# Kernel tuning notes

Hardware: AMD Instinct MI355X
Metric: run time of the kernel (lower is better)

## Reference

```python
import jax, jax.numpy as jnp
import numpy as np

N = 50000          # nodes
E = 500000         # edges (before self-loops)
G = 64             # graphs in batch
SC = 96            # scalar features
D = 32             # embedding dim
IN_DIM = SC + 5 * D  # 256
C = 128            # hidden_channels
H1 = 4             # heads in conv1
NUM_CLASSES = 5
V_OP, V_SRC, V_SINK, V_STR, V_PAY = 256, 512, 512, 128, 1024


def setup_inputs() -> dict:
    key = jax.random.key(0)
    ks = jax.random.split(key, 32)
    inp = {}
    inp['x_scalar'] = jax.random.normal(ks[0], (N, SC), jnp.float32)
    inp['x_opcode'] = jax.random.randint(ks[1], (N, 16), 0, V_OP)
    inp['x_source'] = jax.random.randint(ks[2], (N, 8), 0, V_SRC)
    inp['x_sink'] = jax.random.randint(ks[3], (N, 8), 0, V_SINK)
    inp['x_string_manip'] = jax.random.randint(ks[4], (N, 8), 0, V_STR)
    inp['x_payload'] = jax.random.randint(ks[5], (N, 8), 0, V_PAY)
    inp['edge_index'] = jax.random.randint(ks[6], (2, E), 0, N)
    # sorted graph ids with every graph non-empty
    inp['batch'] = (jnp.arange(N) * G) // N
    # learned params
    s = 0.05
    inp['emb_opcode'] = jax.random.normal(ks[7], (V_OP, D), jnp.float32)
    inp['emb_source'] = jax.random.normal(ks[8], (V_SRC, D), jnp.float32)
    inp['emb_sink'] = jax.random.normal(ks[9], (V_SINK, D), jnp.float32)
    inp['emb_string'] = jax.random.normal(ks[10], (V_STR, D), jnp.float32)
    inp['emb_payload'] = jax.random.normal(ks[11], (V_PAY, D), jnp.float32)
    inp['ln_g'] = jnp.ones((IN_DIM,), jnp.float32)
    inp['ln_b'] = jnp.zeros((IN_DIM,), jnp.float32)
    inp['W1'] = jax.random.normal(ks[12], (IN_DIM, H1 * C), jnp.float32) * s
    inp['att_src1'] = jax.random.normal(ks[13], (H1, C), jnp.float32) * s
    inp['att_dst1'] = jax.random.normal(ks[14], (H1, C), jnp.float32) * s
    inp['b1'] = jnp.zeros((H1 * C,), jnp.float32)
    inp['W2'] = jax.random.normal(ks[15], (H1 * C, C), jnp.float32) * s
    inp['att_src2'] = jax.random.normal(ks[16], (1, C), jnp.float32) * s
    inp['att_dst2'] = jax.random.normal(ks[17], (1, C), jnp.float32) * s
    inp['b2'] = jnp.zeros((C,), jnp.float32)
    inp['Wc1'] = jax.random.normal(ks[18], (C, C // 2), jnp.float32) * s
    inp['bc1'] = jnp.zeros((C // 2,), jnp.float32)
    inp['Wc2'] = jax.random.normal(ks[19], (C // 2, NUM_CLASSES), jnp.float32) * s
    inp['bc2'] = jnp.zeros((NUM_CLASSES,), jnp.float32)
    return inp


def _emb_feat(table, idx):
    # masked mean over the list dim; index 0 is padding
    e = table[idx]                                  # [N, L, D]
    mask = (idx != 0)[..., None].astype(e.dtype)    # [N, L, 1]
    return (e * mask).sum(1) / (mask.sum(1) + 1e-9)


def _layernorm(x, g, b, eps=1e-5):
    mu = x.mean(-1, keepdims=True)
    var = ((x - mu) ** 2).mean(-1, keepdims=True)
    return (x - mu) * jax.lax.rsqrt(var + eps) * g + b


def _gat_conv(x, W, att_src, att_dst, bias, src, dst, heads, out_ch, concat):
    n = x.shape[0]
    h = (x @ W).reshape(n, heads, out_ch)              # [N,H,C]
    a_src = (h * att_src).sum(-1)                      # [N,H]
    a_dst = (h * att_dst).sum(-1)                      # [N,H]
    e = jax.nn.leaky_relu(a_src[src] + a_dst[dst], 0.2)  # [E,H]
    m = jax.ops.segment_max(e, dst, num_segments=n)
    e = jnp.exp(e - m[dst])
    denom = jax.ops.segment_sum(e, dst, num_segments=n)
    alpha = e / (denom[dst] + 1e-16)                   # segment softmax over in-edges
    msg = h[src] * alpha[:, :, None]                   # [E,H,C]
    out = jax.ops.segment_sum(msg, dst, num_segments=n)  # [N,H,C]
    out = out.reshape(n, heads * out_ch) if concat else out.mean(1)
    return out + bias


def reference(x_scalar, x_opcode, x_source, x_sink, x_string_manip, x_payload,
              edge_index, batch,
              emb_opcode, emb_source, emb_sink, emb_string, emb_payload,
              ln_g, ln_b, W1, att_src1, att_dst1, b1,
              W2, att_src2, att_dst2, b2, Wc1, bc1, Wc2, bc2):
    n = x_scalar.shape[0]
    feats = jnp.concatenate([
        x_scalar,
        _emb_feat(emb_opcode, x_opcode),
        _emb_feat(emb_source, x_source),
        _emb_feat(emb_sink, x_sink),
        _emb_feat(emb_string, x_string_manip),
        _emb_feat(emb_payload, x_payload),
    ], axis=1)
    feats = _layernorm(feats, ln_g, ln_b)
    # add self loops (PyG GATConv default)
    loop = jnp.arange(n)
    src = jnp.concatenate([edge_index[0], loop])
    dst = jnp.concatenate([edge_index[1], loop])
    x = jax.nn.elu(_gat_conv(feats, W1, att_src1, att_dst1, b1, src, dst, H1, C, True))
    x = jax.nn.elu(_gat_conv(x, W2, att_src2, att_dst2, b2, src, dst, 1, C, True))
    # global max pool per graph (dropout layers are identity at inference)
    xp = jax.ops.segment_max(x, batch, num_segments=G)  # [G,C]
    hcls = jax.nn.relu(xp @ Wc1 + bc1)
    return hcls @ Wc2 + bc2
```

## Files before the change

### kernel.cpp

```cpp
#include <hip/hip_runtime.h>
#include <hip/hip_bf16.h>
#include <float.h>


#define LEAKY(e) ((e) > 0.f ? (e) : 0.2f * (e))
#define POOL_CH 32

typedef _Float16 half8 __attribute__((ext_vector_type(8)));
typedef float floatx4 __attribute__((ext_vector_type(4)));

__device__ __forceinline__ void async_copy16(const _Float16* gsrc,
                                             const _Float16* ldst) {
  __builtin_amdgcn_global_load_lds(
      (const __attribute__((address_space(1))) unsigned int*)gsrc,
      (__attribute__((address_space(3))) unsigned int*)ldst, 16, 0, 0);
}

__global__ __launch_bounds__(256, 4) void setup_kernel(
    const int* __restrict__ e_dst, int* __restrict__ deg, int E, int HB,
    const float* __restrict__ W1, _Float16* __restrict__ Wt1,
    const float* __restrict__ W2, _Float16* __restrict__ Wt2, int TB,
    const float* __restrict__ xs, const int* __restrict__ xo,
    const int* __restrict__ xsrc, const int* __restrict__ xsk,
    const int* __restrict__ xst, const int* __restrict__ xp,
    const float* __restrict__ eo, const float* __restrict__ es,
    const float* __restrict__ ek, const float* __restrict__ et,
    const float* __restrict__ ep, const float* __restrict__ lng,
    const float* __restrict__ lnb, _Float16* __restrict__ feats, int n) {
  int b = blockIdx.x;
  if (b < HB) {
    int t = b * 256 + threadIdx.x;
    if (t < E) atomicAdd(&deg[e_dst[t]], 1);
    return;
  }
  if (b < HB + TB) {
    int t = (b - HB) * 256 + threadIdx.x;
    if (t < 256 * 512) {
      int nn = t / 256, k = t - nn * 256;
      Wt1[t] = (_Float16)W1[(size_t)k * 512 + nn];
    } else {
      int u = t - 256 * 512;
      int nn = u / 512, k = u - nn * 512;
      Wt2[u] = (_Float16)W2[(size_t)k * 128 + nn];
    }
    return;
  }
  int node = (b - HB - TB) * 4 + (threadIdx.x >> 6);
  if (node >= n) return;
  int l = threadIdx.x & 63;

  int myidx = 0;
  if (l < 16)      myidx = xo[node * 16 + l];
  else if (l < 24) myidx = xsrc[node * 8 + (l - 16)];
  else if (l < 32) myidx = xsk[node * 8 + (l - 24)];
  else if (l < 40) myidx = xst[node * 8 + (l - 32)];
  else if (l < 48) myidx = xp[node * 8 + (l - 40)];

  const float* xrow = xs + (size_t)node * 96;
  float v0 = xrow[l];
  float sc = xrow[64 + (l & 31)];
  float v1, v2, v3;
  bool hi = (l >= 32);
  int d = l & 31;

  {
    float s = 0.f, c = 0.f;
#pragma unroll
    for (int j = 0; j < 16; j++) {
      int id = __shfl(myidx, j);
      float v = eo[(size_t)id * 32 + d];
      float msk = (id != 0) ? 1.f : 0.f;
      s = fmaf(v, msk, s);
      c += msk;
    }
    v1 = hi ? (s / (c + 1e-9f)) : sc;
  }
  {
    const float* tab = hi ? ek : es;
    int base = hi ? 24 : 16;
    float s = 0.f, c = 0.f;
#pragma unroll
    for (int j = 0; j < 8; j++) {
      int id = __shfl(myidx, base + j);
      float v = tab[(size_t)id * 32 + d];
      float msk = (id != 0) ? 1.f : 0.f;
      s = fmaf(v, msk, s);
      c += msk;
    }
    v2 = s / (c + 1e-9f);
  }
  {
    const float* tab = hi ? ep : et;
    int base = hi ? 40 : 32;
    float s = 0.f, c = 0.f;
#pragma unroll
    for (int j = 0; j < 8; j++) {
      int id = __shfl(myidx, base + j);
      float v = tab[(size_t)id * 32 + d];
      float msk = (id != 0) ? 1.f : 0.f;
      s = fmaf(v, msk, s);
      c += msk;
    }
    v3 = s / (c + 1e-9f);
  }

  float sum = v0 + v1 + v2 + v3;
  for (int o = 32; o; o >>= 1) sum += __shfl_xor(sum, o);
  float mu = sum * (1.f / 256.f);
  float d0 = v0 - mu, d1 = v1 - mu, d2 = v2 - mu, d3 = v3 - mu;
  float q = d0 * d0 + d1 * d1 + d2 * d2 + d3 * d3;
  for (int o = 32; o; o >>= 1) q += __shfl_xor(q, o);
  float rstd = rsqrtf(q * (1.f / 256.f) + 1e-5f);

  _Float16* frow = feats + (size_t)node * 256;
  frow[l]       = (_Float16)(d0 * rstd * lng[l] + lnb[l]);
  frow[64 + l]  = (_Float16)(d1 * rstd * lng[64 + l] + lnb[64 + l]);
  frow[128 + l] = (_Float16)(d2 * rstd * lng[128 + l] + lnb[128 + l]);
  frow[192 + l] = (_Float16)(d3 * rstd * lng[192 + l] + lnb[192 + l]);
}

__global__ __launch_bounds__(256) void scan_a(const int* __restrict__ deg,
                                              int* __restrict__ rowptr,
                                              int* __restrict__ bsum, int n) {
  __shared__ int sh[256];
  int b = blockIdx.x, t = threadIdx.x;
  int i = b * 256 + t;
  int v = (i < n) ? deg[i] + 1 : 0;
  sh[t] = v;
  __syncthreads();
  int x = v;
  for (int o = 1; o < 256; o <<= 1) {
    int y = (t >= o) ? sh[t - o] : 0;
    __syncthreads();
    x += y;
    sh[t] = x;
    __syncthreads();
  }
  if (i < n) rowptr[i] = x - v;
  if (t == 255) bsum[b] = x;
}

__global__ __launch_bounds__(256) void scan_c(int* __restrict__ rowptr,
                                              int* __restrict__ rowptr_work,
                                              const int* __restrict__ bsum,
                                              int n, int total) {
  int b = blockIdx.x;
  int off = 0;
  for (int j = 0; j < b; j++) off += bsum[j];
  int i = b * 256 + threadIdx.x;
  if (i < n) {
    int r = rowptr[i] + off;
    rowptr[i] = r;
    rowptr_work[i] = r;
  } else if (i == n) {
    rowptr[n] = total;
  }
}

__global__ __launch_bounds__(256) void fill_kernel(
    const int* __restrict__ src, const int* __restrict__ dst,
    const int* __restrict__ rowptr, int* __restrict__ rowptr_work,
    int* __restrict__ csr_src, int E, int n) {
  int t = blockIdx.x * 256 + threadIdx.x;
  if (t < E) {
    int d = dst[t];
    int pos = atomicAdd(&rowptr_work[d], 1);
    csr_src[pos] = src[t];
  } else if (t < E + n) {
    int i = t - E;
    csr_src[rowptr[i + 1] - 1] = i;
  }
}

__global__ __launch_bounds__(256) void gemm_f16_att(
    const _Float16* __restrict__ A, const _Float16* __restrict__ Bt,
    _Float16* __restrict__ C, const float* __restrict__ att_src,
    const float* __restrict__ att_dst, float* __restrict__ a_src_out,
    float* __restrict__ a_dst_out, int astride, int K, int N) {
  __shared__ __attribute__((aligned(16))) _Float16 As[128 * 32];
  __shared__ __attribute__((aligned(16))) _Float16 Bs[128 * 32];
  int m0 = blockIdx.y * 128;
  int n0 = blockIdx.x * 128;
  int tid = threadIdx.x;
  int wave = tid >> 6, lane = tid & 63;
  int wm = (wave >> 1) * 64, wn = (wave & 1) * 64;
  int lr = lane & 15, lq = lane >> 4;
  int wbase = tid & ~63;

  floatx4 acc[4][4] = {};

  for (int k0 = 0; k0 < K; k0 += 32) {
#pragma unroll
    for (int c = 0; c < 2; c++) {
      int sid = c * 256 + tid;
      int row = sid >> 2;
      int cs = (sid & 3) ^ (row & 3);
      const _Float16* ga = A + (size_t)(m0 + row) * K + k0 + cs * 8;
      const _Float16* gb = Bt + (size_t)(n0 + row) * K + k0 + cs * 8;
      async_copy16(ga, As + (size_t)(c * 256 + wbase) * 8);
      async_copy16(gb, Bs + (size_t)(c * 256 + wbase) * 8);
    }
    __syncthreads();

    half8 af[4], bf[4];
#pragma unroll
    for (int i = 0; i < 4; i++) {
      int row = wm + i * 16 + lr;
      af[i] = *(const half8*)(As + ((row << 2) + (lq ^ (row & 3))) * 8);
    }
#pragma unroll
    for (int j = 0; j < 4; j++) {
      int row = wn + j * 16 + lr;
      bf[j] = *(const half8*)(Bs + ((row << 2) + (lq ^ (row & 3))) * 8);
    }
#pragma unroll
    for (int i = 0; i < 4; i++)
#pragma unroll
      for (int j = 0; j < 4; j++)
        acc[i][j] =
            __builtin_amdgcn_mfma_f32_16x16x32_f16(af[i], bf[j], acc[i][j], 0, 0, 0);
    __syncthreads();
  }

#pragma unroll
  for (int i = 0; i < 4; i++) {
    int rbase = m0 + wm + i * 16 + lq * 4;
#pragma unroll
    for (int r = 0; r < 4; r++) {
      int row = rbase + r;
#pragma unroll
      for (int j = 0; j < 4; j++) {
        int col = n0 + wn + j * 16 + lr;
        C[(size_t)row * N + col] = (_Float16)acc[i][j][r];
      }
    }
  }

  float asv[4], adv[4];
#pragma unroll
  for (int j = 0; j < 4; j++) {
    int col = n0 + wn + j * 16 + lr;
    asv[j] = att_src[col];
    adv[j] = att_dst[col];
  }
  float ps[4][4], pd[4][4];
#pragma unroll
  for (int i = 0; i < 4; i++)
#pragma unroll
    for (int r = 0; r < 4; r++) {
      float s = 0.f, d = 0.f;
#pragma unroll
      for (int j = 0; j < 4; j++) {
        s += acc[i][j][r] * asv[j];
        d += acc[i][j][r] * adv[j];
      }
#pragma unroll
      for (int o = 1; o < 16; o <<= 1) {
        s += __shfl_xor(s, o);
        d += __shfl_xor(d, o);
      }
      ps[i][r] = s;
      pd[i][r] = d;
    }
  float* sred = (float*)&As[0];
  if (wn == 64 && lr == 0) {
#pragma unroll
    for (int i = 0; i < 4; i++)
#pragma unroll
      for (int r = 0; r < 4; r++) {
        int rl = wm + i * 16 + lq * 4 + r;
        sred[rl * 2] = ps[i][r];
        sred[rl * 2 + 1] = pd[i][r];
      }
  }
  __syncthreads();
  if (wn == 0 && lr == 0) {
    int hsel = n0 >> 7;
#pragma unroll
    for (int i = 0; i < 4; i++)
#pragma unroll
      for (int r = 0; r < 4; r++) {
        int rl = wm + i * 16 + lq * 4 + r;
        int row = m0 + rl;
        a_src_out[(size_t)row * astride + hsel] = ps[i][r] + sred[rl * 2];
        a_dst_out[(size_t)row * astride + hsel] = pd[i][r] + sred[rl * 2 + 1];
      }
  }
}

__global__ __launch_bounds__(256) void gat1_agg(
    const _Float16* __restrict__ h1, const float* __restrict__ asrc,
    const float* __restrict__ adst, const int* __restrict__ rowptr,
    const int* __restrict__ csr_src, const float* __restrict__ bias,
    _Float16* __restrict__ out, int n) {
  int node = blockIdx.x * 4 + (threadIdx.x >> 6);
  if (node >= n) return;
  int l = threadIdx.x & 63;
  int hh = l >> 4;
  int li = l & 15;
  int r0 = rowptr[node];
  int deg = rowptr[node + 1] - r0;
  int cb = l * 8;

  float acc[8] = {};

  if (deg <= 64) {
    float adm = adst[node * 4 + hh];
    int s_reg[4];
    float ww[4];
    float m = -1e30f;
#pragma unroll
    for (int c = 0; c < 4; c++) {
      int k = c * 16 + li;
      int s = (k < deg) ? csr_src[r0 + k] : -1;
      s_reg[c] = s;
      float e = -1e30f;
      if (s >= 0) {
        float t = asrc[(size_t)s * 4 + hh] + adm;
        e = LEAKY(t);
      }
      ww[c] = e;
      m = fmaxf(m, e);
    }
#pragma unroll
    for (int o = 1; o < 16; o <<= 1) m = fmaxf(m, __shfl_xor(m, o));
    float sum = 0.f;
#pragma unroll
    for (int c = 0; c < 4; c++) {
      float w = (s_reg[c] >= 0) ? __expf(ww[c] - m) : 0.f;
      ww[c] = w;
      sum += w;
    }
#pragma unroll
    for (int o = 1; o < 16; o <<= 1) sum += __shfl_xor(sum, o);
    float sinv = 1.f / (sum + 1e-16f);
#pragma unroll
    for (int c = 0; c < 4; c++) ww[c] *= sinv;

#pragma unroll
    for (int c = 0; c < 4; c++) {
      int base = c * 16;
      if (base >= deg) break;
      int lim = min(16, deg - base);
      int jl = 0;
      for (; jl + 4 <= lim; jl += 4) {
        int s0 = __shfl(s_reg[c], jl);
        int s1 = __shfl(s_reg[c], jl + 1);
        int s2 = __shfl(s_reg[c], jl + 2);
        int s3 = __shfl(s_reg[c], jl + 3);
        float w0 = __shfl(ww[c], hh * 16 + jl);
        float w1 = __shfl(ww[c], hh * 16 + jl + 1);
        float w2 = __shfl(ww[c], hh * 16 + jl + 2);
        float w3 = __shfl(ww[c], hh * 16 + jl + 3);
        const half8 hv0 = *(const half8*)(h1 + (size_t)s0 * 512 + cb);
        const half8 hv1 = *(const half8*)(h1 + (size_t)s1 * 512 + cb);
        const half8 hv2 = *(const half8*)(h1 + (size_t)s2 * 512 + cb);
        const half8 hv3 = *(const half8*)(h1 + (size_t)s3 * 512 + cb);
#pragma unroll
        for (int q = 0; q < 8; q++)
          acc[q] += w0 * (float)hv0[q] + w1 * (float)hv1[q] +
                    w2 * (float)hv2[q] + w3 * (float)hv3[q];
      }
      for (; jl < lim; jl++) {
        int s0 = __shfl(s_reg[c], jl);
        float w0 = __shfl(ww[c], hh * 16 + jl);
        const half8 hv0 = *(const half8*)(h1 + (size_t)s0 * 512 + cb);
#pragma unroll
        for (int q = 0; q < 8; q++) acc[q] += w0 * (float)hv0[q];
      }
    }
  } else {
    float4 ad4 = *(const float4*)(adst + node * 4);
    float adv[4] = {ad4.x, ad4.y, ad4.z, ad4.w};
    float m[4] = {-1e30f, -1e30f, -1e30f, -1e30f};
    for (int k = l; k < deg; k += 64) {
      int s = csr_src[r0 + k];
      float4 av = *(const float4*)(asrc + (size_t)s * 4);
      float e;
      e = LEAKY(av.x + adv[0]); m[0] = fmaxf(m[0], e);
      e = LEAKY(av.y + adv[1]); m[1] = fmaxf(m[1], e);
      e = LEAKY(av.z + adv[2]); m[2] = fmaxf(m[2], e);
      e = LEAKY(av.w + adv[3]); m[3] = fmaxf(m[3], e);
    }
    for (int o = 1; o < 64; o <<= 1) {
#pragma unroll
      for (int h = 0; h < 4; h++) m[h] = fmaxf(m[h], __shfl_xor(m[h], o));
    }
    float sum[4] = {0.f, 0.f, 0.f, 0.f};
    for (int k = l; k < deg; k += 64) {
      int s = csr_src[r0 + k];
      float4 av = *(const float4*)(asrc + (size_t)s * 4);
      float e;
      e = LEAKY(av.x + adv[0]); sum[0] += __expf(e - m[0]);
      e = LEAKY(av.y + adv[1]); sum[1] += __expf(e - m[1]);
      e = LEAKY(av.z + adv[2]); sum[2] += __expf(e - m[2]);
      e = LEAKY(av.w + adv[3]); sum[3] += __expf(e - m[3]);
    }
    for (int o = 1; o < 64; o <<= 1) {
#pragma unroll
      for (int h = 0; h < 4; h++) sum[h] += __shfl_xor(sum[h], o);
    }
    float mm = m[hh];
    float sinv = 1.f / (sum[hh] + 1e-16f);
    float adm = adv[hh];
    for (int k = 0; k < deg; k++) {
      int s = csr_src[r0 + k];
      float a = asrc[(size_t)s * 4 + hh];
      float e = LEAKY(a + adm);
      float w = __expf(e - mm) * sinv;
      const half8 hv = *(const half8*)(h1 + (size_t)s * 512 + cb);
#pragma unroll
      for (int q = 0; q < 8; q++) acc[q] += w * (float)hv[q];
    }
  }

  const float* bp = bias + cb;
  half8 ov;
#pragma unroll
  for (int j = 0; j < 8; j++) {
    float r = acc[j] + bp[j];
    ov[j] = (_Float16)(r > 0.f ? r : (__expf(r) - 1.f));
  }
  *(half8*)(out + (size_t)node * 512 + cb) = ov;
}

__global__ __launch_bounds__(256) void gat2_agg(
    const _Float16* __restrict__ h2, const float* __restrict__ asrc,
    const float* __restrict__ adst, const int* __restrict__ rowptr,
    const int* __restrict__ csr_src, const float* __restrict__ bias,
    _Float16* __restrict__ out, int n) {
  int node = blockIdx.x * 4 + (threadIdx.x >> 6);
  if (node >= n) return;
  int l = threadIdx.x & 63;
  int r0 = rowptr[node];
  int deg = rowptr[node + 1] - r0;

  if (deg <= 64) {
    float ad = adst[node];
    int s = (l < deg) ? csr_src[r0 + l] : -1;
    float e = -1e30f;
    if (s >= 0) {
      float t = asrc[s] + ad;
      e = LEAKY(t);
    }
    float m = e;
    for (int o = 1; o < 64; o <<= 1) m = fmaxf(m, __shfl_xor(m, o));
    float w = (s >= 0) ? __expf(e - m) : 0.f;
    float sum = w;
    for (int o = 1; o < 64; o <<= 1) sum += __shfl_xor(sum, o);
    w *= 1.f / (sum + 1e-16f);

    int g4 = l >> 4;
    int ch = (l & 15) * 8;
    float acc[8] = {};
    for (int j = 0; j < deg; j += 4) {
      int je = j + g4;
      int jc = min(je, 63);
      int sj = __shfl(s, jc);
      float wj = (je < deg) ? __shfl(w, jc) : 0.f;
      if (sj < 0) sj = 0;
      const half8 hv = *(const half8*)(h2 + (size_t)sj * 128 + ch);
#pragma unroll
      for (int q = 0; q < 8; q++) acc[q] += wj * (float)hv[q];
    }
#pragma unroll
    for (int q = 0; q < 8; q++) {
      acc[q] += __shfl_xor(acc[q], 16);
      acc[q] += __shfl_xor(acc[q], 32);
    }
    if (l < 16) {
      half8 ov;
#pragma unroll
      for (int q = 0; q < 8; q++) {
        float r = acc[q] + bias[ch + q];
        ov[q] = (_Float16)(r > 0.f ? r : (__expf(r) - 1.f));
      }
      *(half8*)(out + (size_t)node * 128 + ch) = ov;
    }
  } else {
    float ad = adst[node];
    float m = -1e30f;
    for (int k = l; k < deg; k += 64) {
      int s = csr_src[r0 + k];
      float e = LEAKY(asrc[s] + ad);
      m = fmaxf(m, e);
    }
    for (int o = 1; o < 64; o <<= 1) m = fmaxf(m, __shfl_xor(m, o));
    float sum = 0.f;
    for (int k = l; k < deg; k += 64) {
      int s = csr_src[r0 + k];
      float e = LEAKY(asrc[s] + ad);
      sum += __expf(e - m);
    }
    for (int o = 1; o < 64; o <<= 1) sum += __shfl_xor(sum, o);
    float sinv = 1.f / (sum + 1e-16f);
    int cb = l * 2;
    float a0 = 0.f, a1 = 0.f;
    for (int k = 0; k < deg; k++) {
      int s = csr_src[r0 + k];
      float e = LEAKY(asrc[s] + ad);
      float w = __expf(e - m) * sinv;
      const _Float16* hp = h2 + (size_t)s * 128 + cb;
      a0 += w * (float)hp[0];
      a1 += w * (float)hp[1];
    }
    float ra = a0 + bias[cb];
    float rb = a1 + bias[cb + 1];
    out[(size_t)node * 128 + cb]     = (_Float16)(ra > 0.f ? ra : (__expf(ra) - 1.f));
    out[(size_t)node * 128 + cb + 1] = (_Float16)(rb > 0.f ? rb : (__expf(rb) - 1.f));
  }
}

__device__ inline int lower_bound_i(const int* a, int n, int v) {
  int lo = 0, hi = n;
  while (lo < hi) {
    int mid = (lo + hi) >> 1;
    if (a[mid] < v) lo = mid + 1; else hi = mid;
  }
  return lo;
}

__global__ __launch_bounds__(128) void pool_partial(
    const _Float16* __restrict__ x2, const int* __restrict__ batch,
    float* __restrict__ partial, int n) {
  int g = blockIdx.y;
  int j = blockIdx.x;
  int t = threadIdx.x;
  int start = lower_bound_i(batch, n, g);
  int end = lower_bound_i(batch, n, g + 1);
  int len = end - start;
  int c0 = start + (int)((long long)len * j / POOL_CH);
  int c1 = start + (int)((long long)len * (j + 1) / POOL_CH);
  float m = -FLT_MAX;
  for (int i = c0; i < c1; i++) m = fmaxf(m, (float)x2[(size_t)i * 128 + t]);
  partial[((size_t)g * POOL_CH + j) * 128 + t] = m;
}

__global__ __launch_bounds__(128) void pool_final(
    const float* __restrict__ partial, float* __restrict__ pool) {
  int g = blockIdx.x;
  int t = threadIdx.x;
  float m = -FLT_MAX;
#pragma unroll
  for (int j = 0; j < POOL_CH; j++)
    m = fmaxf(m, partial[((size_t)g * POOL_CH + j) * 128 + t]);
  pool[g * 128 + t] = m;
}

__global__ __launch_bounds__(64) void classifier_kernel(
    const float* __restrict__ pool, const float* __restrict__ Wc1,
    const float* __restrict__ bc1, const float* __restrict__ Wc2,
    const float* __restrict__ bc2, float* __restrict__ out) {
  int g = blockIdx.x;
  int t = threadIdx.x;
  __shared__ float xp[128];
  __shared__ float hc[64];
  xp[t] = pool[g * 128 + t];
  xp[t + 64] = pool[g * 128 + 64 + t];
  __syncthreads();
  float s = bc1[t];
  for (int k = 0; k < 128; k++) s += xp[k] * Wc1[k * 64 + t];
  hc[t] = s > 0.f ? s : 0.f;
  __syncthreads();
  if (t < 5) {
    float o = bc2[t];
    for (int j = 0; j < 64; j++) o += hc[j] * Wc2[j * 5 + t];
    out[g * 5 + t] = o;
  }
}

extern "C" void kernel_launch(void* const* d_in, const int* in_sizes, int n_in,
                              void* d_out, int out_size, void* d_ws, size_t ws_size,
                              hipStream_t stream) {
  const float* x_scalar = (const float*)d_in[0];
  const int* x_opcode = (const int*)d_in[1];
  const int* x_source = (const int*)d_in[2];
  const int* x_sink = (const int*)d_in[3];
  const int* x_string = (const int*)d_in[4];
  const int* x_payload = (const int*)d_in[5];
  const int* edge_index = (const int*)d_in[6];
  const int* batch = (const int*)d_in[7];
  const float* emb_opcode = (const float*)d_in[8];
  const float* emb_source = (const float*)d_in[9];
  const float* emb_sink = (const float*)d_in[10];
  const float* emb_string = (const float*)d_in[11];
  const float* emb_payload = (const float*)d_in[12];
  const float* ln_g = (const float*)d_in[13];
  const float* ln_b = (const float*)d_in[14];
  const float* W1 = (const float*)d_in[15];
  const float* att_src1 = (const float*)d_in[16];
  const float* att_dst1 = (const float*)d_in[17];
  const float* b1 = (const float*)d_in[18];
  const float* W2 = (const float*)d_in[19];
  const float* att_src2 = (const float*)d_in[20];
  const float* att_dst2 = (const float*)d_in[21];
  const float* b2 = (const float*)d_in[22];
  const float* Wc1 = (const float*)d_in[23];
  const float* bc1 = (const float*)d_in[24];
  const float* Wc2 = (const float*)d_in[25];
  const float* bc2 = (const float*)d_in[26];
  float* out = (float*)d_out;

  const int N = in_sizes[0] / 96;
  const int E = in_sizes[6] / 2;
  const int G = out_size / 5;
  const int Npad = (N + 127) / 128 * 128;

  const int* e_src = edge_index;
  const int* e_dst = edge_index + E;

  char* w = (char*)d_ws;
  size_t o = 0;
  auto take = [&](size_t bytes) -> void* {
    void* p = w + o;
    o += (bytes + 255) & ~(size_t)255;
    return p;
  };
  char* regionA = (char*)take((size_t)Npad * 256 * 2);
  char* regionB = (char*)take((size_t)Npad * 512 * 2);
  _Float16* x1 = (_Float16*)take((size_t)Npad * 512 * 2);
  _Float16* Wt1 = (_Float16*)take((size_t)512 * 256 * 2);
  _Float16* Wt2 = (_Float16*)take((size_t)128 * 512 * 2);
  float* a_src1 = (float*)take((size_t)Npad * 4 * 4);
  float* a_dst1 = (float*)take((size_t)Npad * 4 * 4);
  float* a_src2 = (float*)take((size_t)Npad * 4);
  float* a_dst2 = (float*)take((size_t)Npad * 4);
  int* deg = (int*)take((size_t)N * 4);
  int* rowptr = (int*)take((size_t)(N + 1) * 4);
  int* rowptr_work = (int*)take((size_t)N * 4);
  int* csr_src = (int*)take((size_t)(E + N) * 4);
  int* bsum = (int*)take(256 * 4);

  _Float16* feats = (_Float16*)regionA;
  _Float16* h2 = (_Float16*)regionA;
  float* partial = (float*)(regionA + (((size_t)Npad * 128 * 2 + 255) & ~(size_t)255));
  float* pool = partial + (size_t)G * POOL_CH * 128;
  _Float16* h1 = (_Float16*)regionB;
  _Float16* x2 = (_Float16*)regionB;

  hipMemsetAsync(deg, 0, (size_t)N * 4, stream);

  int HB = (E + 255) / 256;
  int TB = (256 * 512 + 512 * 128 + 255) / 256;
  int FB = (N + 3) / 4;
  setup_kernel<<<HB + TB + FB, 256, 0, stream>>>(
      e_dst, deg, E, HB, W1, Wt1, W2, Wt2, TB, x_scalar, x_opcode, x_source,
      x_sink, x_string, x_payload, emb_opcode, emb_source, emb_sink, emb_string,
      emb_payload, ln_g, ln_b, feats, N);

  int nb = (N + 255) / 256;
  scan_a<<<nb, 256, 0, stream>>>(deg, rowptr, bsum, N);
  scan_c<<<(N + 256) / 256, 256, 0, stream>>>(rowptr, rowptr_work, bsum, N, E + N);

  fill_kernel<<<(E + N + 255) / 256, 256, 0, stream>>>(e_src, e_dst, rowptr,
                                                       rowptr_work, csr_src, E, N);

  int mblocks = Npad / 128;
  gemm_f16_att<<<dim3(512 / 128, mblocks), 256, 0, stream>>>(
      feats, Wt1, h1, att_src1, att_dst1, a_src1, a_dst1, 4, 256, 512);
  gat1_agg<<<(N + 3) / 4, 256, 0, stream>>>(h1, a_src1, a_dst1, rowptr, csr_src,
                                            b1, x1, N);
  gemm_f16_att<<<dim3(128 / 128, mblocks), 256, 0, stream>>>(
      x1, Wt2, h2, att_src2, att_dst2, a_src2, a_dst2, 1, 512, 128);
  gat2_agg<<<(N + 3) / 4, 256, 0, stream>>>(h2, a_src2, a_dst2, rowptr, csr_src,
                                            b2, x2, N);
  pool_partial<<<dim3(POOL_CH, G), 128, 0, stream>>>(x2, batch, partial, N);
  pool_final<<<G, 128, 0, stream>>>(partial, pool);
  classifier_kernel<<<G, 64, 0, stream>>>(pool, Wc1, bc1, Wc2, bc2, out);
}
```

Baseline: 417.6 us.

## Fuse CSR fill into first GEMM launch and tile weight transposes through LDS

```diff
diff --git a/kernel.cpp b/kernel.cpp
--- a/kernel.cpp
+++ b/kernel.cpp
@@ -19,7 +19,7 @@
 __global__ __launch_bounds__(256, 4) void setup_kernel(
     const int* __restrict__ e_dst, int* __restrict__ deg, int E, int HB,
     const float* __restrict__ W1, _Float16* __restrict__ Wt1,
-    const float* __restrict__ W2, _Float16* __restrict__ Wt2, int TB,
+    const float* __restrict__ W2, _Float16* __restrict__ Wt2,
     const float* __restrict__ xs, const int* __restrict__ xo,
     const int* __restrict__ xsrc, const int* __restrict__ xsk,
     const int* __restrict__ xst, const int* __restrict__ xp,
@@ -27,27 +27,50 @@
     const float* __restrict__ ek, const float* __restrict__ et,
     const float* __restrict__ ep, const float* __restrict__ lng,
     const float* __restrict__ lnb, _Float16* __restrict__ feats, int n) {
+  __shared__ float tl[64][65];
   int b = blockIdx.x;
+  int t = threadIdx.x;
   if (b < HB) {
-    int t = b * 256 + threadIdx.x;
-    if (t < E) atomicAdd(&deg[e_dst[t]], 1);
+    int i = b * 256 + t;
+    if (i < E) atomicAdd(&deg[e_dst[i]], 1);
     return;
   }
-  if (b < HB + TB) {
-    int t = (b - HB) * 256 + threadIdx.x;
-    if (t < 256 * 512) {
-      int nn = t / 256, k = t - nn * 256;
-      Wt1[t] = (_Float16)W1[(size_t)k * 512 + nn];
+  if (b < HB + 48) {
+    int tt = b - HB;
+    int tr = t >> 6, tc = t & 63;
+    if (tt < 32) {
+      int k0 = (tt & 3) * 64, n0 = (tt >> 2) * 64;
+#pragma unroll
+      for (int r = 0; r < 16; r++) {
+        int kr = tr + r * 4;
+        tl[kr][tc] = W1[(size_t)(k0 + kr) * 512 + n0 + tc];
+      }
+      __syncthreads();
+#pragma unroll
+      for (int r = 0; r < 16; r++) {
+        int nr = tr + r * 4;
+        Wt1[(size_t)(n0 + nr) * 256 + k0 + tc] = (_Float16)tl[tc][nr];
+      }
     } else {
-      int u = t - 256 * 512;
-      int nn = u / 512, k = u - nn * 512;
-      Wt2[u] = (_Float16)W2[(size_t)k * 128 + nn];
+      int tt2 = tt - 32;
+      int k0 = (tt2 & 7) * 64, n0 = (tt2 >> 3) * 64;
+#pragma unroll
+      for (int r = 0; r < 16; r++) {
+        int kr = tr + r * 4;
+        tl[kr][tc] = W2[(size_t)(k0 + kr) * 128 + n0 + tc];
+      }
+      __syncthreads();
+#pragma unroll
+      for (int r = 0; r < 16; r++) {
+        int nr = tr + r * 4;
+        Wt2[(size_t)(n0 + nr) * 512 + k0 + tc] = (_Float16)tl[tc][nr];
+      }
     }
     return;
   }
-  int node = (b - HB - TB) * 4 + (threadIdx.x >> 6);
+  int node = (b - HB - 48) * 4 + (t >> 6);
   if (node >= n) return;
-  int l = threadIdx.x & 63;
+  int l = t & 63;
 
   int myidx = 0;
   if (l < 16)      myidx = xo[node * 16 + l];
@@ -157,31 +180,33 @@
   }
 }
 
-__global__ __launch_bounds__(256) void fill_kernel(
-    const int* __restrict__ src, const int* __restrict__ dst,
-    const int* __restrict__ rowptr, int* __restrict__ rowptr_work,
-    int* __restrict__ csr_src, int E, int n) {
-  int t = blockIdx.x * 256 + threadIdx.x;
-  if (t < E) {
-    int d = dst[t];
-    int pos = atomicAdd(&rowptr_work[d], 1);
-    csr_src[pos] = src[t];
-  } else if (t < E + n) {
-    int i = t - E;
-    csr_src[rowptr[i + 1] - 1] = i;
-  }
-}
-
 __global__ __launch_bounds__(256) void gemm_f16_att(
     const _Float16* __restrict__ A, const _Float16* __restrict__ Bt,
     _Float16* __restrict__ C, const float* __restrict__ att_src,
     const float* __restrict__ att_dst, float* __restrict__ a_src_out,
-    float* __restrict__ a_dst_out, int astride, int K, int N) {
+    float* __restrict__ a_dst_out, int astride, int K, int N, int mrows,
+    const int* __restrict__ fsrc, const int* __restrict__ fdst,
+    const int* __restrict__ rowptr, int* __restrict__ rowptr_work,
+    int* __restrict__ csr_src, int fE, int fn) {
   __shared__ __attribute__((aligned(16))) _Float16 As[128 * 32];
   __shared__ __attribute__((aligned(16))) _Float16 Bs[128 * 32];
+  int tid = threadIdx.x;
+
+  if ((int)blockIdx.y >= mrows) {
+    int t = (((int)blockIdx.y - mrows) * gridDim.x + blockIdx.x) * 256 + tid;
+    if (t < fE) {
+      int d = fdst[t];
+      int pos = atomicAdd(&rowptr_work[d], 1);
+      csr_src[pos] = fsrc[t];
+    } else if (t < fE + fn) {
+      int i = t - fE;
+      csr_src[rowptr[i + 1] - 1] = i;
+    }
+    return;
+  }
+
   int m0 = blockIdx.y * 128;
   int n0 = blockIdx.x * 128;
-  int tid = threadIdx.x;
   int wave = tid >> 6, lane = tid & 63;
   int wm = (wave >> 1) * 64, wn = (wave & 1) * 64;
   int lr = lane & 15, lq = lane >> 4;
@@ -641,10 +666,9 @@
   hipMemsetAsync(deg, 0, (size_t)N * 4, stream);
 
   int HB = (E + 255) / 256;
-  int TB = (256 * 512 + 512 * 128 + 255) / 256;
   int FB = (N + 3) / 4;
-  setup_kernel<<<HB + TB + FB, 256, 0, stream>>>(
-      e_dst, deg, E, HB, W1, Wt1, W2, Wt2, TB, x_scalar, x_opcode, x_source,
+  setup_kernel<<<HB + 48 + FB, 256, 0, stream>>>(
+      e_dst, deg, E, HB, W1, Wt1, W2, Wt2, x_scalar, x_opcode, x_source,
       x_sink, x_string, x_payload, emb_opcode, emb_source, emb_sink, emb_string,
       emb_payload, ln_g, ln_b, feats, N);
 
@@ -652,16 +676,16 @@
   scan_a<<<nb, 256, 0, stream>>>(deg, rowptr, bsum, N);
   scan_c<<<(N + 256) / 256, 256, 0, stream>>>(rowptr, rowptr_work, bsum, N, E + N);
 
-  fill_kernel<<<(E + N + 255) / 256, 256, 0, stream>>>(e_src, e_dst, rowptr,
-                                                       rowptr_work, csr_src, E, N);
-
   int mblocks = Npad / 128;
-  gemm_f16_att<<<dim3(512 / 128, mblocks), 256, 0, stream>>>(
-      feats, Wt1, h1, att_src1, att_dst1, a_src1, a_dst1, 4, 256, 512);
+  int fill_rows = (E + N + 4 * 256 - 1) / (4 * 256);
+  gemm_f16_att<<<dim3(4, mblocks + fill_rows), 256, 0, stream>>>(
+      feats, Wt1, h1, att_src1, att_dst1, a_src1, a_dst1, 4, 256, 512, mblocks,
+      e_src, e_dst, rowptr, rowptr_work, csr_src, E, N);
   gat1_agg<<<(N + 3) / 4, 256, 0, stream>>>(h1, a_src1, a_dst1, rowptr, csr_src,
                                             b1, x1, N);
-  gemm_f16_att<<<dim3(128 / 128, mblocks), 256, 0, stream>>>(
-      x1, Wt2, h2, att_src2, att_dst2, a_src2, a_dst2, 1, 512, 128);
+  gemm_f16_att<<<dim3(1, mblocks), 256, 0, stream>>>(
+      x1, Wt2, h2, att_src2, att_dst2, a_src2, a_dst2, 1, 512, 128, mblocks,
+      nullptr, nullptr, nullptr, nullptr, nullptr, 0, 0);
   gat2_agg<<<(N + 3) / 4, 256, 0, stream>>>(h2, a_src2, a_dst2, rowptr, csr_src,
                                             b2, x2, N);
   pool_partial<<<dim3(POOL_CH, G), 128, 0, stream>>>(x2, batch, partial, N);
```

Measured after the change: 399.6 us. 4.3% less time.
